# Kernel optimization log

Hardware: AMD Instinct MI355X
Metric: run time of the kernel (lower is better)

Reference implementation:

```python
import jax, jax.numpy as jnp
import numpy as np

B, C, H, W = 4096, 1, 64, 64
NCLASS = 10
ALPHA = 1.0
EPS = 1e-8  # torch CosineSimilarity eps


def setup_inputs() -> dict:
    key = jax.random.key(0)
    k1, k2, k3 = jax.random.split(key, 3)
    outputs = jax.random.normal(k1, (B, NCLASS), dtype=jnp.float32)
    grad = jax.random.normal(k2, (B, C, H, W), dtype=jnp.float32)
    y = jax.random.randint(k3, (B,), 0, NCLASS)
    return {"outputs": outputs, "grad": grad, "y": y}


def reference(outputs, grad, y):
    b = grad.shape[0]
    # per-sample min-max normalization over all of (C,H,W)
    flat = grad.reshape(b, -1)                      # [B, C*H*W]
    gmax = flat.max(axis=1, keepdims=True)
    gmin = flat.min(axis=1, keepdims=True)
    ngrad = (flat - gmin) / (gmax - gmin)           # [B, D]

    # batched pairwise cosine similarity: normalize + matmul
    norms = jnp.linalg.norm(ngrad, axis=1, keepdims=True)
    vn = ngrad / jnp.maximum(norms, EPS)
    sim = vn @ vn.T                                 # [B, B]

    # pairs (i<j) with the same predicted class (argmax(softmax(o)) == argmax(o))
    pred = jnp.argmax(outputs, axis=1)
    same = pred[:, None] == pred[None, :]
    upper = jnp.triu(jnp.ones((b, b), dtype=bool), k=1)
    mask = same & upper
    xloss = jnp.sum(jnp.where(mask, 1.0 - sim, 0.0)) / b

    # cross-entropy
    logp = jax.nn.log_softmax(outputs, axis=1)
    celoss = -jnp.take_along_axis(logp, y[:, None], axis=1).sum() / b
    return celoss + ALPHA * xloss
```

## Files before the change

kernel.cpp:

```cpp
#include <hip/hip_runtime.h>
#include <math.h>

constexpr int Dn = 4096;
constexpr int Bn = 4096;
constexpr int NCLS = 10;

constexpr int OFF_CUR   = 0;
constexpr int OFF_CE    = 10;
constexpr int OFF_XS    = 11;
constexpr int OFF_NCH   = 12;
constexpr int OFF_DONE  = 13;
constexpr int OFF_CHS   = 16;
constexpr int OFF_ORD   = 32;
constexpr int OFF_CHMAP = 41000;
constexpr int OFF_P     = 41472;

__global__ __launch_bounds__(1024) void pass0_ce_order_sched(
    const float* __restrict__ outputs, const int* __restrict__ y,
    float* __restrict__ ws, int CH)
{
    const int t = threadIdx.x;
    const int w = t >> 6, lane = t & 63;
    int* wsi = (int*)ws;

    __shared__ int whist[16][NCLS];
    __shared__ int wbase[16][NCLS];
    __shared__ int cnt[NCLS];
    __shared__ float sce[16];
    __shared__ unsigned short srec[Bn];

    if (t < 16 * NCLS) ((int*)whist)[t] = 0;
    __syncthreads();

    float ce_acc = 0.f;
    #pragma unroll
    for (int r = 0; r < 4; ++r) {
        const int i = r * 1024 + t;
        const float* o = outputs + (size_t)i * NCLS;
        float m = o[0]; int am = 0;
        #pragma unroll
        for (int k = 1; k < NCLS; ++k) { float ok = o[k]; if (ok > m) { m = ok; am = k; } }
        float se = 0.f;
        #pragma unroll
        for (int k = 0; k < NCLS; ++k) se += expf(o[k] - m);
        ce_acc += m + logf(se) - o[y[i]];

        int myrank = 0, mycnt = 0;
        #pragma unroll
        for (int c = 0; c < NCLS; ++c) {
            unsigned long long mk = __ballot(am == c);
            if (am == c) myrank = __popcll(mk & ((1ull << lane) - 1ull));
            if (lane == c) mycnt = (int)__popcll(mk);
        }
        int localpos = whist[w][am] + myrank;
        if (lane < NCLS) whist[w][lane] += mycnt;
        srec[i] = (unsigned short)((am << 12) | localpos);
    }

    #pragma unroll
    for (int off = 32; off; off >>= 1) ce_acc += __shfl_down(ce_acc, off, 64);
    if (lane == 0) sce[w] = ce_acc;
    __syncthreads();

    if (t < NCLS) {
        int s = 0;
        for (int w2 = 0; w2 < 16; ++w2) { wbase[w2][t] = s; s += whist[w2][t]; }
        cnt[t] = s;
    }
    __syncthreads();

    if (t == 0) {
        float cs = 0.f;
        for (int w2 = 0; w2 < 16; ++w2) cs += sce[w2];
        ws[OFF_CE] = cs;
        int nch = 0;
        for (int c = 0; c < NCLS; ++c) {
            wsi[OFF_CUR + c] = cnt[c];
            wsi[OFF_CHS + c] = nch;
            for (int s = 0; s < cnt[c]; s += CH)
                wsi[OFF_CHMAP + nch++] = (c << 16) | s;
        }
        wsi[OFF_CHS + NCLS] = nch;
        wsi[OFF_NCH] = nch;
    }
    __syncthreads();

    #pragma unroll
    for (int r = 0; r < 4; ++r) {
        const int i = r * 1024 + t;
        unsigned short rec = srec[i];
        int am = rec >> 12, lp = rec & 0xFFF;
        wsi[OFF_ORD + am * Bn + wbase[w][am] + lp] = i;
    }
}

__global__ __launch_bounds__(256) void pass12_fused(
    const float* __restrict__ grad, float* __restrict__ ws, int CH)
{
    const int* wsi = (const int*)ws;
    const int chunk = blockIdx.x;
    if (chunk >= wsi[OFF_NCH]) return;

    const int t = threadIdx.x;
    const int w = t >> 6, lane = t & 63;

    const int e  = wsi[OFF_CHMAP + chunk];
    const int c  = e >> 16;
    const int s0 = e & 0xFFFF;
    const int m  = min(CH, wsi[OFF_CUR + c] - s0);

    float4 acc[16];
    #pragma unroll
    for (int k = 0; k < 16; ++k) acc[k] = make_float4(0.f, 0.f, 0.f, 0.f);
    float sb = 0.f;

    const float4* g4 = (const float4*)grad;
    for (int r = w; r < m; r += 4) {
        const int idx = wsi[OFF_ORD + c * Bn + s0 + r];
        const float4* row = g4 + (size_t)idx * (Dn / 4);
        float4 v[16];
        #pragma unroll
        for (int k = 0; k < 16; ++k) v[k] = row[k * 64 + lane];

        float mn = fminf(fminf(v[0].x, v[0].y), fminf(v[0].z, v[0].w));
        #pragma unroll
        for (int k = 1; k < 16; ++k)
            mn = fminf(mn, fminf(fminf(v[k].x, v[k].y), fminf(v[k].z, v[k].w)));
        #pragma unroll
        for (int off = 1; off < 64; off <<= 1)
            mn = fminf(mn, __shfl_xor(mn, off, 64));

        float ss = 0.f;
        #pragma unroll
        for (int k = 0; k < 16; ++k) {
            float dx = v[k].x - mn, dy = v[k].y - mn;
            float dz = v[k].z - mn, dw = v[k].w - mn;
            ss += dx * dx + dy * dy + dz * dz + dw * dw;
        }
        #pragma unroll
        for (int off = 1; off < 64; off <<= 1)
            ss += __shfl_xor(ss, off, 64);

        const float a = 1.0f / sqrtf(ss);
        sb += -mn * a;
        #pragma unroll
        for (int k = 0; k < 16; ++k) {
            acc[k].x = fmaf(v[k].x, a, acc[k].x);
            acc[k].y = fmaf(v[k].y, a, acc[k].y);
            acc[k].z = fmaf(v[k].z, a, acc[k].z);
            acc[k].w = fmaf(v[k].w, a, acc[k].w);
        }
    }
    #pragma unroll
    for (int k = 0; k < 16; ++k) {
        acc[k].x += sb; acc[k].y += sb; acc[k].z += sb; acc[k].w += sb;
    }

    __shared__ float4 sacc[Dn / 4];
    if (w == 0) {
        #pragma unroll
        for (int k = 0; k < 16; ++k) sacc[k * 64 + lane] = acc[k];
    }
    __syncthreads();
    #pragma unroll
    for (int ww = 1; ww < 4; ++ww) {
        if (w == ww) {
            #pragma unroll
            for (int k = 0; k < 16; ++k) {
                float4 s = sacc[k * 64 + lane];
                s.x += acc[k].x; s.y += acc[k].y; s.z += acc[k].z; s.w += acc[k].w;
                sacc[k * 64 + lane] = s;
            }
        }
        __syncthreads();
    }
    float4* Pc = (float4*)(ws + OFF_P) + (size_t)chunk * (Dn / 4);
    #pragma unroll
    for (int k = 0; k < 4; ++k) Pc[k * 256 + t] = sacc[k * 256 + t];
}

__global__ __launch_bounds__(256) void pass34_final(
    float* __restrict__ ws, float* __restrict__ out)
{
    const int t = threadIdx.x;
    const int idx = blockIdx.x * 256 + t;
    const int c = idx >> 12;
    const int j = idx & (Dn - 1);
    const int w = t >> 6, lane = t & 63;
    const int* wsi = (const int*)ws;

    const int cs  = wsi[OFF_CHS + c];
    const int ce2 = wsi[OFF_CHS + c + 1];
    const float* P = ws + OFF_P;

    float s = 0.f;
    for (int ch = cs; ch < ce2; ++ch)
        s += P[(size_t)ch * Dn + j];
    float p = s * s;

    #pragma unroll
    for (int off = 32; off; off >>= 1) p += __shfl_down(p, off, 64);
    __shared__ float sr[4];
    if (lane == 0) sr[w] = p;
    __syncthreads();
    if (t == 0) {
        atomicAdd(&ws[OFF_XS], sr[0] + sr[1] + sr[2] + sr[3]);
        __threadfence();
        int ticket = atomicAdd(&((int*)ws)[OFF_DONE], 1);
        if (ticket == (NCLS * Dn / 256) - 1) {
            float xs = atomicAdd(&ws[OFF_XS], 0.0f);
            const int* n = wsi + OFF_CUR;
            double n2 = 0.0;
            #pragma unroll
            for (int k = 0; k < NCLS; ++k) { double nc = (double)n[k]; n2 += nc * nc; }
            double xloss = (n2 - (double)xs) / (2.0 * (double)Bn);
            double celoss = (double)ws[OFF_CE] / (double)Bn;
            out[0] = (float)(celoss + xloss);
        }
    }
}

extern "C" void kernel_launch(void* const* d_in, const int* in_sizes, int n_in,
                              void* d_out, int out_size, void* d_ws, size_t ws_size,
                              hipStream_t stream)
{
    const float* outputs = (const float*)d_in[0];
    const float* grad    = (const float*)d_in[1];
    const int*   y       = (const int*)d_in[2];
    float* ws  = (float*)d_ws;
    float* out = (float*)d_out;

    const size_t availf = ws_size / sizeof(float);
    const int cands[6] = {16, 32, 64, 128, 256, 512};
    int CH = 512, maxch = Bn / 512 + NCLS;
    for (int k = 0; k < 6; ++k) {
        int mc = Bn / cands[k] + NCLS;
        size_t need = (size_t)OFF_P + (size_t)mc * Dn;
        if (need <= availf) { CH = cands[k]; maxch = mc; break; }
    }

    hipMemsetAsync(d_ws, 0, 128, stream);
    pass0_ce_order_sched<<<1, 1024, 0, stream>>>(outputs, y, ws, CH);
    pass12_fused<<<maxch, 256, 0, stream>>>(grad, ws, CH);
    pass34_final<<<NCLS * Dn / 256, 256, 0, stream>>>(ws, out);
}
```

Before: 132.8 us.

## Parallelize class bucketing and shrink chunks to one row per wave

The single-block pass that computes cross-entropy and groups rows by predicted class becomes a 16-block kernel using shared and global atomics. The grad pass now uses a fixed chunk of 4 rows, one per wave, so about 1034 blocks run instead of the few chosen by workspace size. Chunk boundaries are recomputed from class counts rather than read from a precomputed chunk map. The aims are to remove the serial single-block prologue and spread the memory-bound normalization over more CUs. In exchange, the partial-sum buffer and final reduction grow, and row order within a class is no longer deterministic.

```diff
diff --git a/kernel.cpp b/kernel.cpp
--- a/kernel.cpp
+++ b/kernel.cpp
@@ -4,121 +4,78 @@
 constexpr int Dn = 4096;
 constexpr int Bn = 4096;
 constexpr int NCLS = 10;
-
-constexpr int OFF_CUR   = 0;
-constexpr int OFF_CE    = 10;
-constexpr int OFF_XS    = 11;
-constexpr int OFF_NCH   = 12;
-constexpr int OFF_DONE  = 13;
-constexpr int OFF_CHS   = 16;
-constexpr int OFF_ORD   = 32;
-constexpr int OFF_CHMAP = 41000;
-constexpr int OFF_P     = 41472;
-
-__global__ __launch_bounds__(1024) void pass0_ce_order_sched(
+constexpr int CH = 4;
+constexpr int MAXCH = Bn / CH + NCLS;
+
+constexpr int OFF_CUR  = 0;
+constexpr int OFF_CE   = 10;
+constexpr int OFF_XS   = 11;
+constexpr int OFF_DONE = 12;
+constexpr int OFF_ORD  = 16;
+constexpr int OFF_P    = 41024;
+
+__global__ __launch_bounds__(256) void pass0_ce_order(
     const float* __restrict__ outputs, const int* __restrict__ y,
-    float* __restrict__ ws, int CH)
+    float* __restrict__ ws)
 {
     const int t = threadIdx.x;
+    const int i = blockIdx.x * 256 + t;
     const int w = t >> 6, lane = t & 63;
     int* wsi = (int*)ws;
 
-    __shared__ int whist[16][NCLS];
-    __shared__ int wbase[16][NCLS];
-    __shared__ int cnt[NCLS];
-    __shared__ float sce[16];
-    __shared__ unsigned short srec[Bn];
-
-    if (t < 16 * NCLS) ((int*)whist)[t] = 0;
-    __syncthreads();
-
-    float ce_acc = 0.f;
-    #pragma unroll
-    for (int r = 0; r < 4; ++r) {
-        const int i = r * 1024 + t;
-        const float* o = outputs + (size_t)i * NCLS;
-        float m = o[0]; int am = 0;
-        #pragma unroll
-        for (int k = 1; k < NCLS; ++k) { float ok = o[k]; if (ok > m) { m = ok; am = k; } }
-        float se = 0.f;
-        #pragma unroll
-        for (int k = 0; k < NCLS; ++k) se += expf(o[k] - m);
-        ce_acc += m + logf(se) - o[y[i]];
-
-        int myrank = 0, mycnt = 0;
-        #pragma unroll
-        for (int c = 0; c < NCLS; ++c) {
-            unsigned long long mk = __ballot(am == c);
-            if (am == c) myrank = __popcll(mk & ((1ull << lane) - 1ull));
-            if (lane == c) mycnt = (int)__popcll(mk);
-        }
-        int localpos = whist[w][am] + myrank;
-        if (lane < NCLS) whist[w][lane] += mycnt;
-        srec[i] = (unsigned short)((am << 12) | localpos);
-    }
-
-    #pragma unroll
-    for (int off = 32; off; off >>= 1) ce_acc += __shfl_down(ce_acc, off, 64);
-    if (lane == 0) sce[w] = ce_acc;
-    __syncthreads();
-
-    if (t < NCLS) {
-        int s = 0;
-        for (int w2 = 0; w2 < 16; ++w2) { wbase[w2][t] = s; s += whist[w2][t]; }
-        cnt[t] = s;
-    }
-    __syncthreads();
-
-    if (t == 0) {
-        float cs = 0.f;
-        for (int w2 = 0; w2 < 16; ++w2) cs += sce[w2];
-        ws[OFF_CE] = cs;
-        int nch = 0;
-        for (int c = 0; c < NCLS; ++c) {
-            wsi[OFF_CUR + c] = cnt[c];
-            wsi[OFF_CHS + c] = nch;
-            for (int s = 0; s < cnt[c]; s += CH)
-                wsi[OFF_CHMAP + nch++] = (c << 16) | s;
-        }
-        wsi[OFF_CHS + NCLS] = nch;
-        wsi[OFF_NCH] = nch;
-    }
-    __syncthreads();
-
-    #pragma unroll
-    for (int r = 0; r < 4; ++r) {
-        const int i = r * 1024 + t;
-        unsigned short rec = srec[i];
-        int am = rec >> 12, lp = rec & 0xFFF;
-        wsi[OFF_ORD + am * Bn + wbase[w][am] + lp] = i;
-    }
+    __shared__ int hist[NCLS];
+    __shared__ int lbase[NCLS];
+    __shared__ float sce[4];
+    if (t < NCLS) hist[t] = 0;
+    __syncthreads();
+
+    const float* o = outputs + (size_t)i * NCLS;
+    float m = o[0]; int am = 0;
+    #pragma unroll
+    for (int k = 1; k < NCLS; ++k) { float ok = o[k]; if (ok > m) { m = ok; am = k; } }
+    float se = 0.f;
+    #pragma unroll
+    for (int k = 0; k < NCLS; ++k) se += expf(o[k] - m);
+    float ce = m + logf(se) - o[y[i]];
+
+    int rank = atomicAdd(&hist[am], 1);
+
+    #pragma unroll
+    for (int off = 32; off; off >>= 1) ce += __shfl_down(ce, off, 64);
+    if (lane == 0) sce[w] = ce;
+    __syncthreads();
+
+    if (t < NCLS) lbase[t] = atomicAdd(&wsi[OFF_CUR + t], hist[t]);
+    if (t == 0) atomicAdd(&ws[OFF_CE], sce[0] + sce[1] + sce[2] + sce[3]);
+    __syncthreads();
+
+    wsi[OFF_ORD + am * Bn + lbase[am] + rank] = i;
 }
 
 __global__ __launch_bounds__(256) void pass12_fused(
-    const float* __restrict__ grad, float* __restrict__ ws, int CH)
+    const float* __restrict__ grad, float* __restrict__ ws)
 {
     const int* wsi = (const int*)ws;
-    const int chunk = blockIdx.x;
-    if (chunk >= wsi[OFF_NCH]) return;
-
-    const int t = threadIdx.x;
-    const int w = t >> 6, lane = t & 63;
-
-    const int e  = wsi[OFF_CHMAP + chunk];
-    const int c  = e >> 16;
-    const int s0 = e & 0xFFFF;
-    const int m  = min(CH, wsi[OFF_CUR + c] - s0);
-
-    float4 acc[16];
-    #pragma unroll
-    for (int k = 0; k < 16; ++k) acc[k] = make_float4(0.f, 0.f, 0.f, 0.f);
-    float sb = 0.f;
-
-    const float4* g4 = (const float4*)grad;
-    for (int r = w; r < m; r += 4) {
-        const int idx = wsi[OFF_ORD + c * Bn + s0 + r];
-        const float4* row = g4 + (size_t)idx * (Dn / 4);
-        float4 v[16];
+    const int t = threadIdx.x, w = t >> 6, lane = t & 63;
+
+    int c = -1, s0 = 0, cnt = 0;
+    {
+        int b = (int)blockIdx.x, acc = 0;
+        #pragma unroll
+        for (int k = 0; k < NCLS; ++k) {
+            int n = wsi[OFF_CUR + k];
+            int nch = (n + CH - 1) / CH;
+            if (c < 0 && b < acc + nch) { c = k; s0 = (b - acc) * CH; cnt = n; }
+            acc += nch;
+        }
+    }
+    if (c < 0) return;
+    const int m = min(CH, cnt - s0);
+
+    float4 v[16];
+    if (w < m) {
+        const int idx = wsi[OFF_ORD + c * Bn + s0 + w];
+        const float4* row = (const float4*)grad + (size_t)idx * (Dn / 4);
         #pragma unroll
         for (int k = 0; k < 16; ++k) v[k] = row[k * 64 + lane];
 
@@ -142,41 +99,55 @@
             ss += __shfl_xor(ss, off, 64);
 
         const float a = 1.0f / sqrtf(ss);
-        sb += -mn * a;
-        #pragma unroll
-        for (int k = 0; k < 16; ++k) {
-            acc[k].x = fmaf(v[k].x, a, acc[k].x);
-            acc[k].y = fmaf(v[k].y, a, acc[k].y);
-            acc[k].z = fmaf(v[k].z, a, acc[k].z);
-            acc[k].w = fmaf(v[k].w, a, acc[k].w);
-        }
-    }
-    #pragma unroll
-    for (int k = 0; k < 16; ++k) {
-        acc[k].x += sb; acc[k].y += sb; acc[k].z += sb; acc[k].w += sb;
-    }
-
-    __shared__ float4 sacc[Dn / 4];
+        const float b = -mn * a;
+        #pragma unroll
+        for (int k = 0; k < 16; ++k) {
+            v[k].x = fmaf(v[k].x, a, b);
+            v[k].y = fmaf(v[k].y, a, b);
+            v[k].z = fmaf(v[k].z, a, b);
+            v[k].w = fmaf(v[k].w, a, b);
+        }
+    } else {
+        #pragma unroll
+        for (int k = 0; k < 16; ++k) v[k] = make_float4(0.f, 0.f, 0.f, 0.f);
+    }
+
+    __shared__ float4 buf0[1024];
+    __shared__ float4 buf1[1024];
+    if (w == 2) {
+        #pragma unroll
+        for (int k = 0; k < 16; ++k) buf0[k * 64 + lane] = v[k];
+    }
+    if (w == 3) {
+        #pragma unroll
+        for (int k = 0; k < 16; ++k) buf1[k * 64 + lane] = v[k];
+    }
+    __syncthreads();
     if (w == 0) {
         #pragma unroll
-        for (int k = 0; k < 16; ++k) sacc[k * 64 + lane] = acc[k];
-    }
-    __syncthreads();
-    #pragma unroll
-    for (int ww = 1; ww < 4; ++ww) {
-        if (w == ww) {
-            #pragma unroll
-            for (int k = 0; k < 16; ++k) {
-                float4 s = sacc[k * 64 + lane];
-                s.x += acc[k].x; s.y += acc[k].y; s.z += acc[k].z; s.w += acc[k].w;
-                sacc[k * 64 + lane] = s;
-            }
-        }
-        __syncthreads();
-    }
-    float4* Pc = (float4*)(ws + OFF_P) + (size_t)chunk * (Dn / 4);
-    #pragma unroll
-    for (int k = 0; k < 4; ++k) Pc[k * 256 + t] = sacc[k * 256 + t];
+        for (int k = 0; k < 16; ++k) {
+            float4 u = buf0[k * 64 + lane];
+            v[k].x += u.x; v[k].y += u.y; v[k].z += u.z; v[k].w += u.w;
+        }
+    }
+    if (w == 1) {
+        #pragma unroll
+        for (int k = 0; k < 16; ++k) {
+            float4 u = buf1[k * 64 + lane];
+            v[k].x += u.x; v[k].y += u.y; v[k].z += u.z; v[k].w += u.w;
+            buf1[k * 64 + lane] = v[k];
+        }
+    }
+    __syncthreads();
+    if (w == 0) {
+        float4* Pc = (float4*)(ws + OFF_P) + (size_t)blockIdx.x * (Dn / 4);
+        #pragma unroll
+        for (int k = 0; k < 16; ++k) {
+            float4 u = buf1[k * 64 + lane];
+            v[k].x += u.x; v[k].y += u.y; v[k].z += u.z; v[k].w += u.w;
+            Pc[k * 64 + lane] = v[k];
+        }
+    }
 }
 
 __global__ __launch_bounds__(256) void pass34_final(
@@ -189,13 +160,24 @@
     const int w = t >> 6, lane = t & 63;
     const int* wsi = (const int*)ws;
 
-    const int cs  = wsi[OFF_CHS + c];
-    const int ce2 = wsi[OFF_CHS + c + 1];
+    int cs = 0, ce2 = 0;
+    {
+        int acc = 0;
+        #pragma unroll
+        for (int k = 0; k < NCLS; ++k) {
+            int nch = (wsi[OFF_CUR + k] + CH - 1) / CH;
+            if (k == c) { cs = acc; ce2 = acc + nch; }
+            acc += nch;
+        }
+    }
+
     const float* P = ws + OFF_P;
-
     float s = 0.f;
-    for (int ch = cs; ch < ce2; ++ch)
-        s += P[(size_t)ch * Dn + j];
+    int ch = cs;
+    for (; ch + 4 <= ce2; ch += 4)
+        s += P[(size_t)(ch + 0) * Dn + j] + P[(size_t)(ch + 1) * Dn + j]
+           + P[(size_t)(ch + 2) * Dn + j] + P[(size_t)(ch + 3) * Dn + j];
+    for (; ch < ce2; ++ch) s += P[(size_t)ch * Dn + j];
     float p = s * s;
 
     #pragma unroll
@@ -230,17 +212,8 @@
     float* ws  = (float*)d_ws;
     float* out = (float*)d_out;
 
-    const size_t availf = ws_size / sizeof(float);
-    const int cands[6] = {16, 32, 64, 128, 256, 512};
-    int CH = 512, maxch = Bn / 512 + NCLS;
-    for (int k = 0; k < 6; ++k) {
-        int mc = Bn / cands[k] + NCLS;
-        size_t need = (size_t)OFF_P + (size_t)mc * Dn;
-        if (need <= availf) { CH = cands[k]; maxch = mc; break; }
-    }
-
-    hipMemsetAsync(d_ws, 0, 128, stream);
-    pass0_ce_order_sched<<<1, 1024, 0, stream>>>(outputs, y, ws, CH);
-    pass12_fused<<<maxch, 256, 0, stream>>>(grad, ws, CH);
+    hipMemsetAsync(d_ws, 0, 64, stream);
+    pass0_ce_order<<<Bn / 256, 256, 0, stream>>>(outputs, y, ws);
+    pass12_fused<<<MAXCH, 256, 0, stream>>>(grad, ws);
     pass34_final<<<NCLS * Dn / 256, 256, 0, stream>>>(ws, out);
 }
```

Measured after the change: 118.4 us. 1.12x faster.
